# Kernel tuning notes

Hardware: AMD Instinct MI355X
Metric: run time of the kernel (lower is better)

Reference implementation:

```python
import jax, jax.numpy as jnp
import numpy as np


def setup_inputs() -> dict:
    key = jax.random.key(0)
    T, B, E, F = 128, 4, 10000, 16
    x = jax.random.normal(key, (T, B, E, F), dtype=jnp.float32)
    return {"x": x, "dummy_index": 0}


def reference(x, dummy_index):
    # x: [time, batch, element, feature]
    d = dummy_index
    # f: all features except the time column -> [T, B, E, F-1]
    f = jnp.concatenate([x[..., :d], x[..., d + 1:]], axis=-1)
    # t: the time coordinate column -> [T, B, E, 1]
    t = x[..., d:d + 1]
    # _diff: reflect-pad left by 1 (pad value = t[1]) then negate the pad,
    # so dt[0] = t[0] - (-t[1]) = t[0] + t[1], dt[i] = t[i] - t[i-1] for i >= 1
    dt0 = t[0] + t[1]                 # [B, E, 1]
    dt_rest = t[1:] - t[:-1]          # [T-1, B, E, 1]
    dt = jnp.concatenate([dt0[None], dt_rest], axis=0)  # [T, B, E, 1]
    # trapezoid-like accumulation: multiply, prefix-sum over time, activation
    integrated = jnp.cumsum(f * dt, axis=0)  # [T, B, E, F-1]
    return jnp.tanh(integrated)
```

## Files before the change

kernel.cpp:

```cpp
#include <hip/hip_runtime.h>


#define TT   128
#define BE   40000
#define X4_T 160000
#define O_T  600000

__device__ __forceinline__ float fast_tanh(float x) {
  float e = __expf(2.0f * x);
  return 1.0f - __fdividef(2.0f, e + 1.0f);
}

__global__ __launch_bounds__(256) void integ_kernel(const float* __restrict__ x,
                                                    float* __restrict__ out) {
  const int gid  = blockIdx.x * 256 + threadIdx.x;
  const int idx  = gid >> 2;
  const int sub  = gid & 3;
  const int lane = threadIdx.x & 63;
  const int srcl = lane & ~3;

  const float4* xv = reinterpret_cast<const float4*>(x) + ((size_t)idx * 4 + sub);
  float* ob = out + (size_t)idx * 15 + (4 * sub - 1);

  float4 v0 = xv[0];
  float4 v1 = xv[(size_t)X4_T];
  float t0 = __shfl(v0.x, srcl, 64);
  float t1 = __shfl(v1.x, srcl, 64);

  float dt = t0 + t1;
  float a0 = v0.x * dt;
  float a1 = v0.y * dt;
  float a2 = v0.z * dt;
  float a3 = v0.w * dt;
  if (sub) ob[0] = fast_tanh(a0);
  ob[1] = fast_tanh(a1);
  ob[2] = fast_tanh(a2);
  ob[3] = fast_tanh(a3);

  float tprev = t0;
  float4 v = v1;
  for (int t = 1; t < TT; ++t) {
    int tn = t + 1 < TT ? t + 1 : TT - 1;
    float4 vn = xv[(size_t)tn * X4_T];

    float tc = __shfl(v.x, srcl, 64);
    dt = tc - tprev;
    a0 = fmaf(v.x, dt, a0);
    a1 = fmaf(v.y, dt, a1);
    a2 = fmaf(v.z, dt, a2);
    a3 = fmaf(v.w, dt, a3);

    float* o = ob + (size_t)t * O_T;
    if (sub) o[0] = fast_tanh(a0);
    o[1] = fast_tanh(a1);
    o[2] = fast_tanh(a2);
    o[3] = fast_tanh(a3);

    tprev = tc;
    v = vn;
  }
}

extern "C" void kernel_launch(void* const* d_in, const int* in_sizes, int n_in,
                              void* d_out, int out_size, void* d_ws, size_t ws_size,
                              hipStream_t stream) {
  const float* x = (const float*)d_in[0];
  float* out = (float*)d_out;
  integ_kernel<<<dim3(625), dim3(256), 0, stream>>>(x, out);
}
```

Before: 524.1 us.

## Prefetch eight timesteps per chunk, use nontemporal stores, and 64-thread blocks

Restructures the time loop to load a chunk of eight timesteps ahead into registers, so more global loads are in flight per thread and memory latency is better hidden. Output stores become nontemporal to avoid polluting caches with streaming data. Blocks shrink to a single wavefront with four times as many blocks, for finer-grained scheduling. The cost is higher register pressure from holding two eight-entry float4 arrays.

```diff
diff --git a/kernel.cpp b/kernel.cpp
--- a/kernel.cpp
+++ b/kernel.cpp
@@ -2,7 +2,7 @@
 
 
 #define TT   128
-#define BE   40000
+#define CH   8
 #define X4_T 160000
 #define O_T  600000
 
@@ -11,9 +11,9 @@
   return 1.0f - __fdividef(2.0f, e + 1.0f);
 }
 
-__global__ __launch_bounds__(256) void integ_kernel(const float* __restrict__ x,
-                                                    float* __restrict__ out) {
-  const int gid  = blockIdx.x * 256 + threadIdx.x;
+__global__ __launch_bounds__(64) void integ_kernel(const float* __restrict__ x,
+                                                   float* __restrict__ out) {
+  const int gid  = blockIdx.x * 64 + threadIdx.x;
   const int idx  = gid >> 2;
   const int sub  = gid & 3;
   const int lane = threadIdx.x & 63;
@@ -22,42 +22,45 @@
   const float4* xv = reinterpret_cast<const float4*>(x) + ((size_t)idx * 4 + sub);
   float* ob = out + (size_t)idx * 15 + (4 * sub - 1);
 
-  float4 v0 = xv[0];
-  float4 v1 = xv[(size_t)X4_T];
-  float t0 = __shfl(v0.x, srcl, 64);
-  float t1 = __shfl(v1.x, srcl, 64);
+  float4 cur[CH], nxt[CH];
+#pragma unroll
+  for (int i = 0; i < CH; ++i) cur[i] = xv[(size_t)i * X4_T];
 
-  float dt = t0 + t1;
-  float a0 = v0.x * dt;
-  float a1 = v0.y * dt;
-  float a2 = v0.z * dt;
-  float a3 = v0.w * dt;
-  if (sub) ob[0] = fast_tanh(a0);
-  ob[1] = fast_tanh(a1);
-  ob[2] = fast_tanh(a2);
-  ob[3] = fast_tanh(a3);
+  float a0 = 0.f, a1 = 0.f, a2 = 0.f, a3 = 0.f;
+  float tprev = 0.f;
 
-  float tprev = t0;
-  float4 v = v1;
-  for (int t = 1; t < TT; ++t) {
-    int tn = t + 1 < TT ? t + 1 : TT - 1;
-    float4 vn = xv[(size_t)tn * X4_T];
+  for (int tb = 0; tb < TT; tb += CH) {
+#pragma unroll
+    for (int i = 0; i < CH; ++i) {
+      int tn = tb + CH + i;
+      if (tn > TT - 1) tn = TT - 1;
+      nxt[i] = xv[(size_t)tn * X4_T];
+    }
 
-    float tc = __shfl(v.x, srcl, 64);
-    dt = tc - tprev;
-    a0 = fmaf(v.x, dt, a0);
-    a1 = fmaf(v.y, dt, a1);
-    a2 = fmaf(v.z, dt, a2);
-    a3 = fmaf(v.w, dt, a3);
+    float tc[CH];
+#pragma unroll
+    for (int i = 0; i < CH; ++i) tc[i] = __shfl(cur[i].x, srcl, 64);
 
-    float* o = ob + (size_t)t * O_T;
-    if (sub) o[0] = fast_tanh(a0);
-    o[1] = fast_tanh(a1);
-    o[2] = fast_tanh(a2);
-    o[3] = fast_tanh(a3);
+#pragma unroll
+    for (int i = 0; i < CH; ++i) {
+      const int t = tb + i;
+      const float dt = (t == 0) ? (tc[0] + tc[1]) : (tc[i] - tprev);
+      a0 = fmaf(cur[i].x, dt, a0);
+      a1 = fmaf(cur[i].y, dt, a1);
+      a2 = fmaf(cur[i].z, dt, a2);
+      a3 = fmaf(cur[i].w, dt, a3);
 
-    tprev = tc;
-    v = vn;
+      float* o = ob + (size_t)t * O_T;
+      if (sub) __builtin_nontemporal_store(fast_tanh(a0), o + 0);
+      __builtin_nontemporal_store(fast_tanh(a1), o + 1);
+      __builtin_nontemporal_store(fast_tanh(a2), o + 2);
+      __builtin_nontemporal_store(fast_tanh(a3), o + 3);
+
+      tprev = tc[i];
+    }
+
+#pragma unroll
+    for (int i = 0; i < CH; ++i) cur[i] = nxt[i];
   }
 }
 
@@ -66,5 +69,5 @@
                               hipStream_t stream) {
   const float* x = (const float*)d_in[0];
   float* out = (float*)d_out;
-  integ_kernel<<<dim3(625), dim3(256), 0, stream>>>(x, out);
+  integ_kernel<<<dim3(2500), dim3(64), 0, stream>>>(x, out);
 }
```

New measurement: 617.5 us. 1.18x slower.
